# Kernel optimization log

Measured on AMD Instinct MI355X. Metric: run time of the kernel, lower is better.

Reference implementation:

```python
import jax, jax.numpy as jnp
import numpy as np

ALPHA = 0.2  # LeakyReLU negative slope
NEG_BIG = -9e15

def setup_inputs() -> dict:
    key = jax.random.key(0)
    k1, k2, k3, k4 = jax.random.split(key, 4)
    N, F_in, F_out = 8192, 512, 64
    inp = jax.random.normal(k1, (N, F_in), dtype=jnp.float32)
    adj = jax.random.randint(k2, (N, N), 0, 2, dtype=jnp.int32)
    W = jax.random.normal(k3, (F_in, F_out), dtype=jnp.float32) * (1.414 / np.sqrt(F_in + F_out))
    a = jax.random.normal(k4, (2 * F_out, 1), dtype=jnp.float32) * 0.1
    return {"input": inp, "adj": adj, "W": W, "a": a}

def reference(input, adj, W, a):
    # h: [N, F_out]
    h = input @ W
    F_out = h.shape[1]
    # Decompose a into a1 (source part) and a2 (target part):
    a1 = a[:F_out, 0]   # [F_out]
    a2 = a[F_out:, 0]   # [F_out]
    s1 = h @ a1         # [N]
    s2 = h @ a2         # [N]
    e = s1[:, None] + s2[None, :]                      # [N, N]
    e = jnp.where(e > 0, e, ALPHA * e)                 # LeakyReLU
    e = jnp.where(adj > 0, e, jnp.float32(NEG_BIG))    # mask non-edges
    attention = jax.nn.softmax(e, axis=1)              # [N, N]
    # dropout with p=0.0 / eval mode -> identity
    h_prime = attention @ h                            # [N, F_out]
    return h_prime
```

## Files before the change

### kernel.cpp

```cpp
#include <hip/hip_runtime.h>
#include <hip/hip_bf16.h>

#define ALPHA 0.2f

constexpr int N    = 8192;
constexpr int FIN  = 512;
constexpr int FOUT = 64;
constexpr int NSPLIT = 8;
constexpr int JCHUNK = N / NSPLIT;

typedef __attribute__((ext_vector_type(8))) short short8;
typedef __attribute__((ext_vector_type(4))) float f32x4;

__global__ __launch_bounds__(256) void k1_proj(
    const float* __restrict__ input, const float* __restrict__ W,
    const float* __restrict__ a, __hip_bfloat16* __restrict__ hbT,
    float* __restrict__ s1, float* __restrict__ s2)
{
    __shared__ __hip_bfloat16 tile[8][64];
    const int tid  = threadIdx.x;
    const int col  = tid & 63;
    const int g    = tid >> 6;
    const int rbase = blockIdx.x * 8;

    float acc[2] = {0.f, 0.f};
    const float* in0 = input + (size_t)(rbase + g * 2) * FIN;

    for (int k = 0; k < FIN; k += 8) {
        float w[8];
        #pragma unroll
        for (int q = 0; q < 8; ++q) w[q] = W[(k + q) * FOUT + col];
        const float4 x0a = *(const float4*)(in0 + 0 * FIN + k);
        const float4 x0b = *(const float4*)(in0 + 0 * FIN + k + 4);
        const float4 x1a = *(const float4*)(in0 + 1 * FIN + k);
        const float4 x1b = *(const float4*)(in0 + 1 * FIN + k + 4);
        acc[0] = fmaf(x0a.w, w[3], fmaf(x0a.z, w[2], fmaf(x0a.y, w[1], fmaf(x0a.x, w[0], acc[0]))));
        acc[0] = fmaf(x0b.w, w[7], fmaf(x0b.z, w[6], fmaf(x0b.y, w[5], fmaf(x0b.x, w[4], acc[0]))));
        acc[1] = fmaf(x1a.w, w[3], fmaf(x1a.z, w[2], fmaf(x1a.y, w[1], fmaf(x1a.x, w[0], acc[1]))));
        acc[1] = fmaf(x1b.w, w[7], fmaf(x1b.z, w[6], fmaf(x1b.y, w[5], fmaf(x1b.x, w[4], acc[1]))));
    }

    const float a1c = a[col];
    const float a2c = a[FOUT + col];
    #pragma unroll
    for (int q = 0; q < 2; ++q) {
        float r1 = acc[q] * a1c;
        float r2 = acc[q] * a2c;
        #pragma unroll
        for (int off = 32; off >= 1; off >>= 1) {
            r1 += __shfl_xor(r1, off, 64);
            r2 += __shfl_xor(r2, off, 64);
        }
        if (col == 0) {
            s1[rbase + g * 2 + q] = r1;
            s2[rbase + g * 2 + q] = r2;
        }
        tile[g * 2 + q][col] = __float2bfloat16(acc[q]);
    }
    __syncthreads();

    if (tid < 128) {
        const int c = tid >> 1, part = tid & 1;
        unsigned short v[4];
        #pragma unroll
        for (int u = 0; u < 4; ++u) {
            __hip_bfloat16 hv = tile[part * 4 + u][c];
            v[u] = *reinterpret_cast<unsigned short*>(&hv);
        }
        *(ushort4*)((unsigned short*)hbT + (size_t)c * N + rbase + part * 4) =
            make_ushort4(v[0], v[1], v[2], v[3]);
    }
}

__global__ __launch_bounds__(256) void k2_attn(
    const int* __restrict__ adj,
    const float* __restrict__ s1, const float* __restrict__ s2,
    const unsigned short* __restrict__ hbT,
    float* __restrict__ pAcc, float* __restrict__ pZ)
{
    const int r   = blockIdx.x;
    const int s   = blockIdx.y;
    const int tid = threadIdx.x;
    const int w    = tid >> 6;
    const int lane = tid & 63;
    const int row16 = lane & 15;
    const int quad  = lane >> 4;

    const int i = r * 64 + w * 16 + row16;
    const float s1i = s1[i];
    const int jbeg = s * JCHUNK;
    const int jend = jbeg + JCHUNK;

    f32x4 acc0 = {0.f, 0.f, 0.f, 0.f};
    f32x4 acc1 = {0.f, 0.f, 0.f, 0.f};
    f32x4 acc2 = {0.f, 0.f, 0.f, 0.f};
    f32x4 acc3 = {0.f, 0.f, 0.f, 0.f};
    float zpart = 0.f;

    const int* adjrow = adj + (size_t)i * N;
    const short* hp = (const short*)hbT;

    {
        const int jj = jbeg + quad * 8;
    }
    int jj0 = jbeg + quad * 8;
    int4   cA  = *(const int4*)(adjrow + jj0);
    int4   cB  = *(const int4*)(adjrow + jj0 + 4);
    float4 cSa = *(const float4*)(s2 + jj0);
    float4 cSb = *(const float4*)(s2 + jj0 + 4);

    for (int j0 = jbeg; j0 < jend; j0 += 32) {
        const int jn = ((j0 + 32 < jend) ? (j0 + 32) : jbeg) + quad * 8;
        const int4   nA  = *(const int4*)(adjrow + jn);
        const int4   nB  = *(const int4*)(adjrow + jn + 4);
        const float4 nSa = *(const float4*)(s2 + jn);
        const float4 nSb = *(const float4*)(s2 + jn + 4);

        const int jj = j0 + quad * 8;

        const short8 b0 = *(const short8*)(hp + (size_t)(row16 +  0) * N + jj);
        const short8 b1 = *(const short8*)(hp + (size_t)(row16 + 16) * N + jj);
        const short8 b2 = *(const short8*)(hp + (size_t)(row16 + 32) * N + jj);
        const short8 b3 = *(const short8*)(hp + (size_t)(row16 + 48) * N + jj);

        float s2v[8];
        s2v[0] = cSa.x; s2v[1] = cSa.y; s2v[2] = cSa.z; s2v[3] = cSa.w;
        s2v[4] = cSb.x; s2v[5] = cSb.y; s2v[6] = cSb.z; s2v[7] = cSb.w;
        int av[8];
        av[0] = cA.x; av[1] = cA.y; av[2] = cA.z; av[3] = cA.w;
        av[4] = cB.x; av[5] = cB.y; av[6] = cB.z; av[7] = cB.w;

        short8 afrag;
        #pragma unroll
        for (int j = 0; j < 8; ++j) {
            float e = s1i + s2v[j];
            e = fmaxf(e, ALPHA * e);
            float pv = (av[j] != 0) ? __expf(e) : 0.f;
            __hip_bfloat16 hv = __float2bfloat16(pv);
            zpart += __bfloat162float(hv);
            afrag[j] = *reinterpret_cast<short*>(&hv);
        }

        acc0 = __builtin_amdgcn_mfma_f32_16x16x32_bf16(afrag, b0, acc0, 0, 0, 0);
        acc1 = __builtin_amdgcn_mfma_f32_16x16x32_bf16(afrag, b1, acc1, 0, 0, 0);
        acc2 = __builtin_amdgcn_mfma_f32_16x16x32_bf16(afrag, b2, acc2, 0, 0, 0);
        acc3 = __builtin_amdgcn_mfma_f32_16x16x32_bf16(afrag, b3, acc3, 0, 0, 0);

        cA = nA; cB = nB; cSa = nSa; cSb = nSb;
    }

    zpart += __shfl_xor(zpart, 16, 64);
    zpart += __shfl_xor(zpart, 32, 64);
    if (quad == 0) pZ[(size_t)s * N + i] = zpart;

    float* outp = pAcc + ((size_t)s * N + (size_t)r * 64 + w * 16) * FOUT;
    #pragma unroll
    for (int reg = 0; reg < 4; ++reg) {
        const int row = quad * 4 + reg;
        outp[row * FOUT + ( 0 + row16)] = acc0[reg];
        outp[row * FOUT + (16 + row16)] = acc1[reg];
        outp[row * FOUT + (32 + row16)] = acc2[reg];
        outp[row * FOUT + (48 + row16)] = acc3[reg];
    }
}

__global__ __launch_bounds__(256) void k3_combine(
    const float* __restrict__ pAcc, const float* __restrict__ pZ,
    float* __restrict__ out)
{
    const int idx = blockIdx.x * 256 + threadIdx.x;
    const int i = idx >> 6;
    float num = 0.f, den = 0.f;
    #pragma unroll
    for (int s = 0; s < NSPLIT; ++s) {
        num += pAcc[(size_t)s * N * FOUT + idx];
        den += pZ[(size_t)s * N + i];
    }
    out[idx] = num / den;
}

extern "C" void kernel_launch(void* const* d_in, const int* in_sizes, int n_in,
                              void* d_out, int out_size, void* d_ws, size_t ws_size,
                              hipStream_t stream)
{
    const float* input = (const float*)d_in[0];
    const int*   adj   = (const int*)d_in[1];
    const float* W     = (const float*)d_in[2];
    const float* a     = (const float*)d_in[3];
    float* out = (float*)d_out;

    char* ws = (char*)d_ws;
    __hip_bfloat16* hbT = (__hip_bfloat16*)ws;
    float* s1   = (float*)(ws + (size_t)FOUT * N * 2);
    float* s2   = s1 + N;
    float* pZ   = s2 + N;
    float* pAcc = pZ + (size_t)NSPLIT * N;

    k1_proj<<<N / 8, 256, 0, stream>>>(input, W, a, hbT, s1, s2);

    dim3 g2(N / 64, NSPLIT);
    k2_attn<<<g2, 256, 0, stream>>>(adj, s1, s2, (const unsigned short*)hbT, pAcc, pZ);

    k3_combine<<<(N * FOUT) / 256, 256, 0, stream>>>(pAcc, pZ, out);
}
```

Measured before the change: 485.8 us.

## Pack adjacency into bitmask in a pre-pass and double the j-split

Adds a pre-pass kernel that compresses the int32 adjacency matrix into a per-row bitmask, so the attention kernel reads one 32-bit mask word per 32 columns instead of 32 int32 values. The attention kernel now always computes the exponential and selects it with a mask bit. NSPLIT goes from 8 to 16, and a launch-bounds occupancy hint is added for more parallelism. The full adjacency matrix is still read once by the pack kernel, and the extra kernel, bitmask write and larger partial buffers add traffic and combine work.

```diff
diff --git a/kernel.cpp b/kernel.cpp
--- a/kernel.cpp
+++ b/kernel.cpp
@@ -6,11 +6,41 @@
 constexpr int N    = 8192;
 constexpr int FIN  = 512;
 constexpr int FOUT = 64;
-constexpr int NSPLIT = 8;
+constexpr int NSPLIT = 16;
 constexpr int JCHUNK = N / NSPLIT;
+constexpr int NB     = N / 8;
 
 typedef __attribute__((ext_vector_type(8))) short short8;
 typedef __attribute__((ext_vector_type(4))) float f32x4;
+
+__global__ __launch_bounds__(256) void k0_pack(const int* __restrict__ adj,
+                                               unsigned char* __restrict__ bits)
+{
+    const int lane = threadIdx.x & 63;
+    const int wv   = threadIdx.x >> 6;
+    const int g    = blockIdx.x * 4 + wv;
+    const int i    = g >> 2;
+    const int segb = (g & 3) * 4;
+    const int* row = adj + (size_t)i * N;
+
+    int4 va[8];
+    #pragma unroll
+    for (int u = 0; u < 4; ++u) {
+        const int jb = (segb + u) * 512 + lane * 8;
+        va[2 * u]     = *(const int4*)(row + jb);
+        va[2 * u + 1] = *(const int4*)(row + jb + 4);
+    }
+    #pragma unroll
+    for (int u = 0; u < 4; ++u) {
+        const int4 a = va[2 * u], b = va[2 * u + 1];
+        unsigned int byte =
+            (a.x != 0 ?   1u : 0u) | (a.y != 0 ?   2u : 0u) |
+            (a.z != 0 ?   4u : 0u) | (a.w != 0 ?   8u : 0u) |
+            (b.x != 0 ?  16u : 0u) | (b.y != 0 ?  32u : 0u) |
+            (b.z != 0 ?  64u : 0u) | (b.w != 0 ? 128u : 0u);
+        bits[(size_t)i * NB + (segb + u) * 64 + lane] = (unsigned char)byte;
+    }
+}
 
 __global__ __launch_bounds__(256) void k1_proj(
     const float* __restrict__ input, const float* __restrict__ W,
@@ -72,8 +102,8 @@
     }
 }
 
-__global__ __launch_bounds__(256) void k2_attn(
-    const int* __restrict__ adj,
+__global__ __launch_bounds__(256, 4) void k2_attn(
+    const unsigned char* __restrict__ bits,
     const float* __restrict__ s1, const float* __restrict__ s2,
     const unsigned short* __restrict__ hbT,
     float* __restrict__ pAcc, float* __restrict__ pZ)
@@ -97,45 +127,37 @@
     f32x4 acc3 = {0.f, 0.f, 0.f, 0.f};
     float zpart = 0.f;
 
-    const int* adjrow = adj + (size_t)i * N;
+    const unsigned char* brow = bits + (size_t)i * NB;
     const short* hp = (const short*)hbT;
 
-    {
-        const int jj = jbeg + quad * 8;
-    }
-    int jj0 = jbeg + quad * 8;
-    int4   cA  = *(const int4*)(adjrow + jj0);
-    int4   cB  = *(const int4*)(adjrow + jj0 + 4);
-    float4 cSa = *(const float4*)(s2 + jj0);
-    float4 cSb = *(const float4*)(s2 + jj0 + 4);
+    unsigned int cM = *(const unsigned int*)(brow + (jbeg >> 3));
+    float4 cSa = *(const float4*)(s2 + jbeg + quad * 8);
+    float4 cSb = *(const float4*)(s2 + jbeg + quad * 8 + 4);
 
     for (int j0 = jbeg; j0 < jend; j0 += 32) {
-        const int jn = ((j0 + 32 < jend) ? (j0 + 32) : jbeg) + quad * 8;
-        const int4   nA  = *(const int4*)(adjrow + jn);
-        const int4   nB  = *(const int4*)(adjrow + jn + 4);
-        const float4 nSa = *(const float4*)(s2 + jn);
-        const float4 nSb = *(const float4*)(s2 + jn + 4);
+        const int j0n = (j0 + 32 < jend) ? (j0 + 32) : jbeg;
+        const unsigned int nM = *(const unsigned int*)(brow + (j0n >> 3));
+        const float4 nSa = *(const float4*)(s2 + j0n + quad * 8);
+        const float4 nSb = *(const float4*)(s2 + j0n + quad * 8 + 4);
 
         const int jj = j0 + quad * 8;
-
         const short8 b0 = *(const short8*)(hp + (size_t)(row16 +  0) * N + jj);
         const short8 b1 = *(const short8*)(hp + (size_t)(row16 + 16) * N + jj);
         const short8 b2 = *(const short8*)(hp + (size_t)(row16 + 32) * N + jj);
         const short8 b3 = *(const short8*)(hp + (size_t)(row16 + 48) * N + jj);
 
+        const unsigned int mbyte = (cM >> (8 * quad)) & 0xffu;
         float s2v[8];
         s2v[0] = cSa.x; s2v[1] = cSa.y; s2v[2] = cSa.z; s2v[3] = cSa.w;
         s2v[4] = cSb.x; s2v[5] = cSb.y; s2v[6] = cSb.z; s2v[7] = cSb.w;
-        int av[8];
-        av[0] = cA.x; av[1] = cA.y; av[2] = cA.z; av[3] = cA.w;
-        av[4] = cB.x; av[5] = cB.y; av[6] = cB.z; av[7] = cB.w;
 
         short8 afrag;
         #pragma unroll
         for (int j = 0; j < 8; ++j) {
             float e = s1i + s2v[j];
             e = fmaxf(e, ALPHA * e);
-            float pv = (av[j] != 0) ? __expf(e) : 0.f;
+            float pv = __expf(e);
+            pv = ((mbyte >> j) & 1u) ? pv : 0.f;
             __hip_bfloat16 hv = __float2bfloat16(pv);
             zpart += __bfloat162float(hv);
             afrag[j] = *reinterpret_cast<short*>(&hv);
@@ -146,7 +168,7 @@
         acc2 = __builtin_amdgcn_mfma_f32_16x16x32_bf16(afrag, b2, acc2, 0, 0, 0);
         acc3 = __builtin_amdgcn_mfma_f32_16x16x32_bf16(afrag, b3, acc3, 0, 0, 0);
 
-        cA = nA; cB = nB; cSa = nSa; cSb = nSb;
+        cM = nM; cSa = nSa; cSb = nSb;
     }
 
     zpart += __shfl_xor(zpart, 16, 64);
@@ -195,11 +217,13 @@
     float* s2   = s1 + N;
     float* pZ   = s2 + N;
     float* pAcc = pZ + (size_t)NSPLIT * N;
-
+    unsigned char* bitsP = (unsigned char*)(pAcc + (size_t)NSPLIT * N * FOUT);
+
+    k0_pack<<<8192, 256, 0, stream>>>(adj, bitsP);
     k1_proj<<<N / 8, 256, 0, stream>>>(input, W, a, hbT, s1, s2);
 
     dim3 g2(N / 64, NSPLIT);
-    k2_attn<<<g2, 256, 0, stream>>>(adj, s1, s2, (const unsigned short*)hbT, pAcc, pZ);
+    k2_attn<<<g2, 256, 0, stream>>>(bitsP, s1, s2, (const unsigned short*)hbT, pAcc, pZ);
 
     k3_combine<<<(N * FOUT) / 256, 256, 0, stream>>>(pAcc, pZ, out);
 }
```

Result: slower. 512.8 us (+5.5%).
